# Kernel tuning notes

Measured on AMD Instinct MI355X. Metric: run time of the kernel, lower is better.

## Reference

```python
import jax, jax.numpy as jnp
import numpy as np

NUM_HEADS = 8


def setup_inputs() -> dict:
    key = jax.random.key(0)
    k1, k2, k3 = jax.random.split(key, 3)
    B, N, C = 4, 8448, 512
    x = jax.random.normal(k1, (B, N, C), dtype=jnp.float32)
    w_qkv = jax.random.normal(k2, (3 * C, C), dtype=jnp.float32) * (C ** -0.5)
    w_proj = jax.random.normal(k3, (C, C), dtype=jnp.float32) * (C ** -0.5)
    b_proj = jnp.zeros((C,), dtype=jnp.float32)
    return {"x": x, "w_qkv": w_qkv, "w_proj": w_proj, "b_proj": b_proj, "N_points": 8192}


def reference(x, w_qkv, w_proj, b_proj, N_points):
    B, N, C = x.shape
    H = NUM_HEADS
    hd = C // H
    scale = hd ** -0.5
    N_latent = N - N_points

    qkv = (x @ w_qkv.T).reshape(B, N, 3, H, hd).transpose(2, 0, 3, 1, 4)  # [3,B,H,N,hd]
    q, k, v = qkv[0], qkv[1], qkv[2]
    q_l, k_l, v_l = q[:, :, :N_latent], k[:, :, :N_latent], v[:, :, :N_latent]
    q_p, k_p, v_p = q[:, :, N_latent:], k[:, :, N_latent:], v[:, :, N_latent:]

    # joint cross+self attention for the points
    attn_cross = jnp.einsum('bhpd,bhld->bhpl', q_p, k_l) * scale        # [B,H,P,L]
    attn_self = jnp.sum(q_p * k_p, axis=-1, keepdims=True) * scale      # [B,H,P,1]
    attn_joint = jax.nn.softmax(jnp.concatenate([attn_cross, attn_self], axis=-1), axis=-1)

    sum_cross = jnp.einsum('bhpl,bhld->bhpd', attn_joint[..., :N_latent], v_l)
    sum_self = attn_joint[..., N_latent:] * v_p
    out_points = (sum_cross + sum_self).transpose(0, 2, 1, 3).reshape(B, N_points, C)

    # standard self-attention over latent tokens
    attn_latent = jax.nn.softmax(jnp.einsum('bhqd,bhkd->bhqk', q_l, k_l) * scale, axis=-1)
    out_latent = jnp.einsum('bhqk,bhkd->bhqd', attn_latent, v_l).transpose(0, 2, 1, 3).reshape(B, N_latent, C)

    output = jnp.concatenate([out_latent, out_points], axis=1) @ w_proj.T + b_proj
    attn_mean = attn_joint[..., :-1].mean(axis=1)  # [B,P,L]
    return output, attn_mean
```

## Files before the change

kernel.cpp:

```cpp
#include <hip/hip_runtime.h>

#define BQ 4
#define NH 8
#define NTOK 8448
#define NLAT 256
#define NPTS 8192
#define CDIM 512
#define HD 64
#define SCALE 0.125f

typedef __attribute__((ext_vector_type(8))) short short8b;
typedef __attribute__((ext_vector_type(4))) float f32x4;

static __device__ __forceinline__ float4 ld4(const float* p) { return *(const float4*)p; }

static __device__ __forceinline__ short f2b(float f) {
  union { float f; unsigned u; } c; c.f = f;
  unsigned u = c.u;
  u += ((u >> 16) & 1u) + 0x7fffu;
  return (short)(u >> 16);
}

static __device__ __forceinline__ float b2f(unsigned short u) {
  union { unsigned u; float f; } c; c.u = ((unsigned)u) << 16; return c.f;
}

static __device__ __forceinline__ int cvtpk(float lo, float hi) {
  int r; asm("v_cvt_pk_bf16_f32 %0, %1, %2" : "=v"(r) : "v"(lo), "v"(hi)); return r;
}

static __device__ __forceinline__ void gload_lds16(const unsigned short* g, unsigned short* l) {
  __builtin_amdgcn_global_load_lds((const __attribute__((address_space(1))) void*)g,
                                   (__attribute__((address_space(3))) void*)l, 16, 0, 0);
}

__global__ __launch_bounds__(256) void to_bf16_3(const float* __restrict__ a, unsigned short* __restrict__ ao_, int na8,
                                                 const float* __restrict__ b, unsigned short* __restrict__ bo, int nb8,
                                                 const float* __restrict__ c, unsigned short* __restrict__ co, int nc8) {
  int i = blockIdx.x * 256 + threadIdx.x;
  const float* src; unsigned short* dst; int idx;
  if (i < na8) { src = a; dst = ao_; idx = i; }
  else if (i < na8 + nb8) { src = b; dst = bo; idx = i - na8; }
  else if (i < na8 + nb8 + nc8) { src = c; dst = co; idx = i - na8 - nb8; }
  else return;
  float4 x0 = ld4(src + (size_t)idx * 8);
  float4 x1 = ld4(src + (size_t)idx * 8 + 4);
  short8b r;
  r[0] = f2b(x0.x); r[1] = f2b(x0.y); r[2] = f2b(x0.z); r[3] = f2b(x0.w);
  r[4] = f2b(x1.x); r[5] = f2b(x1.y); r[6] = f2b(x1.z); r[7] = f2b(x1.w);
  *(short8b*)&dst[(size_t)idx * 8] = r;
}

#define STAGE128(PA, PB, kt, s)                                                              \
  do {                                                                                       \
    const int _c = (kt) * 64 + scell;                                                        \
    unsigned short* _d = &lds[(s) * 16384 + t * 8];                                          \
    gload_lds16((PA) + (size_t)(m0 + sr) * CDIM + _c,       _d);                             \
    gload_lds16((PA) + (size_t)(m0 + 32 + sr) * CDIM + _c,  _d + 2048);                      \
    gload_lds16((PA) + (size_t)(m0 + 64 + sr) * CDIM + _c,  _d + 4096);                      \
    gload_lds16((PA) + (size_t)(m0 + 96 + sr) * CDIM + _c,  _d + 6144);                      \
    gload_lds16((PB) + (size_t)(j0 + sr) * CDIM + _c,       _d + 8192);                      \
    gload_lds16((PB) + (size_t)(j0 + 32 + sr) * CDIM + _c,  _d + 10240);                     \
    gload_lds16((PB) + (size_t)(j0 + 64 + sr) * CDIM + _c,  _d + 12288);                     \
    gload_lds16((PB) + (size_t)(j0 + 96 + sr) * CDIM + _c,  _d + 14336);                     \
  } while (0)

#define GEMM128_BODY(PA, PB)                                                                 \
  __shared__ unsigned short lds[32768];                                                      \
  const int fl = blockIdx.y * gridDim.x + blockIdx.x;                                        \
  const int nchunk = (gridDim.x * gridDim.y) >> 3;                                           \
  const int wid = (fl & 7) * nchunk + (fl >> 3);                                             \
  const int m0 = (wid / gridDim.x) * 128;                                                    \
  const int j0 = (wid % gridDim.x) * 128;                                                    \
  const int t = threadIdx.x;                                                                 \
  const int lane = t & 63, wave = t >> 6;                                                    \
  const int wr = wave >> 1, wc = wave & 1;                                                   \
  const int lm = lane & 15, lq = lane >> 4;                                                  \
  const int sr = t >> 3;                                    \
  const int scell = (((t & 7) ^ (sr & 7)) << 3);                                             \
  int offA[4], offB[4];                                                                      \
  _Pragma("unroll")                                                                          \
  for (int mt = 0; mt < 4; ++mt) {                                                           \
    const int RA = wr * 64 + mt * 16 + lm;                                                   \
    offA[mt] = RA * 64 + ((lq ^ (RA & 7)) << 3);                                             \
    const int RB = wc * 64 + mt * 16 + lm;                                                   \
    offB[mt] = 8192 + RB * 64 + ((lq ^ (RB & 7)) << 3);                                      \
  }                                                                                          \
  f32x4 acc[4][4] = {};                                                                      \
  STAGE128(PA, PB, 0, 0);                                                                    \
  STAGE128(PA, PB, 1, 1);                                                                    \
  for (int kt = 0; kt < 8; ++kt) {                                                           \
    const int s = kt & 1;                                                                    \
    if (kt == 7) asm volatile("s_waitcnt vmcnt(0)" ::: "memory");                            \
    else         asm volatile("s_waitcnt vmcnt(8)" ::: "memory");                            \
    __builtin_amdgcn_s_barrier();                                                            \
    const unsigned short* sb = &lds[s * 16384];                                              \
    short8b af[4][2], bf[4][2];                                                              \
    _Pragma("unroll")                                                                        \
    for (int mt = 0; mt < 4; ++mt) {                                                         \
      const int RA = wr * 64 + mt * 16 + lm;                                                 \
      const int RB = wc * 64 + mt * 16 + lm;                                                 \
      af[mt][0] = *(const short8b*)&sb[offA[mt]];                                            \
      af[mt][1] = *(const short8b*)&sb[(RA * 64) + (((4 | lq) ^ (RA & 7)) << 3)];            \
      bf[mt][0] = *(const short8b*)&sb[offB[mt]];                                            \
      bf[mt][1] = *(const short8b*)&sb[8192 + (RB * 64) + (((4 | lq) ^ (RB & 7)) << 3)];     \
    }                                                                                        \
    asm volatile("s_waitcnt lgkmcnt(0)" ::: "memory");                                       \
    __builtin_amdgcn_s_barrier();                                                            \
    __builtin_amdgcn_sched_barrier(0);                                                       \
    if (kt < 6) STAGE128(PA, PB, kt + 2, s);                                                 \
    __builtin_amdgcn_s_setprio(1);                                                           \
    _Pragma("unroll")                                                                        \
    for (int ks = 0; ks < 2; ++ks)                                                           \
      _Pragma("unroll")                                                                      \
      for (int mt = 0; mt < 4; ++mt)                                                         \
        _Pragma("unroll")                                                                    \
        for (int nt = 0; nt < 4; ++nt)                                                       \
          acc[mt][nt] = __builtin_amdgcn_mfma_f32_16x16x32_bf16(af[mt][ks], bf[nt][ks],      \
                                                                acc[mt][nt], 0, 0, 0);       \
    __builtin_amdgcn_s_setprio(0);                                                           \
  }

__global__ __launch_bounds__(256, 2) void qkv_mfma(const unsigned short* __restrict__ xb,
                                                   const unsigned short* __restrict__ wb,
                                                   unsigned short* __restrict__ qo,
                                                   unsigned short* __restrict__ ko,
                                                   unsigned short* __restrict__ vo) {
  GEMM128_BODY(xb, wb)
  const int s_ = j0 >> 9;
  unsigned short* dst = (s_ == 0) ? qo : ((s_ == 1) ? ko : vo);
  const int b = m0 / NTOK;
  const int n0 = m0 % NTOK;
  const int h = ((j0 >> 6) + wc) & 7;
#pragma unroll
  for (int mt = 0; mt < 4; ++mt) {
#pragma unroll
    for (int r = 0; r < 4; ++r) {
      const int n = n0 + wr * 64 + mt * 16 + lq * 4 + r;
      const size_t ob = (((size_t)b * NH + h) * NTOK + n) * HD;
#pragma unroll
      for (int nt = 0; nt < 4; ++nt)
        dst[ob + nt * 16 + lm] = (unsigned short)f2b(acc[mt][nt][r]);
    }
  }
}

__global__ __launch_bounds__(256, 2) void proj_mfma(const unsigned short* __restrict__ ab,
                                                    const unsigned short* __restrict__ wpb,
                                                    const float* __restrict__ bias,
                                                    float* __restrict__ out) {
  GEMM128_BODY(ab, wpb)
#pragma unroll
  for (int mt = 0; mt < 4; ++mt) {
#pragma unroll
    for (int r = 0; r < 4; ++r) {
      const int m = m0 + wr * 64 + mt * 16 + lq * 4 + r;
#pragma unroll
      for (int nt = 0; nt < 4; ++nt) {
        const int j = j0 + wc * 64 + nt * 16 + lm;
        out[(size_t)m * CDIM + j] = acc[mt][nt][r] + bias[j];
      }
    }
  }
}

__global__ __launch_bounds__(512, 2) void points_attn_mfma(const unsigned short* __restrict__ qb,
                                                           const unsigned short* __restrict__ kb,
                                                           const unsigned short* __restrict__ vb,
                                                           unsigned short* __restrict__ aob,
                                                           float* __restrict__ md) {
  __shared__ unsigned short kl[64 * 256];
  __shared__ unsigned short vt[64 * 256];
  const int fl = blockIdx.x;
  const int wid = (fl & 7) * 128 + (fl >> 3);
  const int bh = wid >> 5;
  const int ptile = wid & 31;
  const int t = threadIdx.x;
  const int lane = t & 63, wave = t >> 6;
  const int lm = lane & 15, lq = lane >> 4;
  const size_t bhb = (size_t)bh * NTOK * HD;
  if (t < 256) {
    const unsigned short* krg = kb + bhb + (size_t)t * HD;
    short8b kv[8];
#pragma unroll
    for (int i = 0; i < 8; ++i) kv[i] = *(const short8b*)(krg + i * 8);
    const int mtw = ((t >> 5) << 1) | ((t >> 2) & 1);
    const int lmw = (((t >> 3) & 3) << 2) | (t & 3);
    const int rr = (mtw << 4) | lmw;
#pragma unroll
    for (int j = 0; j < 8; ++j)
      *(short8b*)&kl[rr * 64 + ((j ^ (rr & 7)) << 3)] = kv[j];
  } else {
    const int tt = t - 256;
    const unsigned short* vr = vb + bhb + (size_t)tt * HD;
    short8b rv[8];
#pragma unroll
    for (int i = 0; i < 8; ++i) rv[i] = *(const short8b*)(vr + i * 8);
    const int gsw = tt >> 3, wi = tt & 7;
#pragma unroll
    for (int d0 = 0; d0 < 8; ++d0)
#pragma unroll
      for (int j = 0; j < 8; ++j)
        vt[(d0 * 8 + j) * 256 + ((gsw ^ j) << 3) + wi] = (unsigned short)rv[d0][j];
  }
  __syncthreads();
  const int b = bh >> 3, h = bh & 7;
#pragma unroll 1
  for (int pass = 0; pass < 2; ++pass) {
    const int pp0 = ptile * 256 + wave * 32 + pass * 16;
    const size_t qrow = bhb + (size_t)(NLAT + pp0 + lm) * HD;
    unsigned short vself[4][4];
#pragma unroll
    for (int ntd = 0; ntd < 4; ++ntd)
#pragma unroll
      for (int r = 0; r < 4; ++r)
        vself[ntd][r] = vb[bhb + (size_t)(NLAT + pp0 + lq * 4 + r) * HD + ntd * 16 + lm];
    const short8b bq0 = *(const short8b*)(qb + qrow + lq * 8);
    const short8b bq1 = *(const short8b*)(qb + qrow + 32 + lq * 8);
    f32x4 s[16] = {};
    __builtin_amdgcn_s_setprio(1);
#pragma unroll
    for (int mt = 0; mt < 16; ++mt) {
      const int rr = mt * 16 + lm;
      const short8b ak0 = *(const short8b*)&kl[rr * 64 + ((lq ^ (rr & 7)) << 3)];
      const short8b ak1 = *(const short8b*)&kl[rr * 64 + (((4 | lq) ^ (rr & 7)) << 3)];
      s[mt] = __builtin_amdgcn_mfma_f32_16x16x32_bf16(ak0, bq0, s[mt], 0, 0, 0);
      s[mt] = __builtin_amdgcn_mfma_f32_16x16x32_bf16(ak1, bq1, s[mt], 0, 0, 0);
    }
    __builtin_amdgcn_s_setprio(0);
    float sself = 0.f;
    {
      const unsigned short* qp = qb + qrow + lq * 16;
      const unsigned short* kp = kb + qrow + lq * 16;
      short8b q0 = *(const short8b*)qp, q1 = *(const short8b*)(qp + 8);
      short8b k0 = *(const short8b*)kp, k1 = *(const short8b*)(kp + 8);
#pragma unroll
      for (int j = 0; j < 8; ++j)
        sself += b2f((unsigned short)q0[j]) * b2f((unsigned short)k0[j]) +
                 b2f((unsigned short)q1[j]) * b2f((unsigned short)k1[j]);
    }
    sself += __shfl_xor(sself, 16);
    sself += __shfl_xor(sself, 32);
    sself *= SCALE;
    float mx = -1e30f;
#pragma unroll
    for (int mt = 0; mt < 16; ++mt)
#pragma unroll
      for (int r = 0; r < 4; ++r) mx = fmaxf(mx, s[mt][r]);
    mx = fmaxf(mx, __shfl_xor(mx, 16));
    mx = fmaxf(mx, __shfl_xor(mx, 32));
    const float m = fmaxf(mx * SCALE, sself);
    float sum = 0.f;
#pragma unroll
    for (int mt = 0; mt < 16; ++mt)
#pragma unroll
      for (int r = 0; r < 4; ++r) {
        float e = __expf(fmaf(s[mt][r], SCALE, -m));
        s[mt][r] = e;
        sum += e;
      }
    sum += __shfl_xor(sum, 16);
    sum += __shfl_xor(sum, 32);
    const float pself = __expf(sself - m);
    const float denom = sum + pself;
    if (lq == 0)
      *(float2*)&md[((size_t)bh * NPTS + pp0 + lm) * 2] = make_float2(m, denom);
    f32x4 o[4] = {};
    __builtin_amdgcn_s_setprio(1);
#pragma unroll
    for (int ks = 0; ks < 8; ++ks) {
      union { int i[4]; short8b v; } af;
      af.i[0] = cvtpk(s[2 * ks][0], s[2 * ks][1]);
      af.i[1] = cvtpk(s[2 * ks][2], s[2 * ks][3]);
      af.i[2] = cvtpk(s[2 * ks + 1][0], s[2 * ks + 1][1]);
      af.i[3] = cvtpk(s[2 * ks + 1][2], s[2 * ks + 1][3]);
#pragma unroll
      for (int ntd = 0; ntd < 4; ++ntd) {
        const int row = ntd * 16 + lm;
        const short8b bv = *(const short8b*)&vt[row * 256 + ((((ks << 2) | lq) ^ (lm & 7)) << 3)];
        o[ntd] = __builtin_amdgcn_mfma_f32_16x16x32_bf16(af.v, bv, o[ntd], 0, 0, 0);
      }
    }
    __builtin_amdgcn_s_setprio(0);
    float invd[4], psl[4];
#pragma unroll
    for (int r = 0; r < 4; ++r) {
      const int src = lq * 4 + r;
      invd[r] = 1.f / __shfl(denom, src);
      psl[r] = __shfl(pself, src);
    }
#pragma unroll
    for (int ntd = 0; ntd < 4; ++ntd) {
#pragma unroll
      for (int r = 0; r < 4; ++r) {
        const int n = NLAT + pp0 + lq * 4 + r;
        const float val = (o[ntd][r] + psl[r] * b2f(vself[ntd][r])) * invd[r];
        aob[((size_t)b * NTOK + n) * CDIM + h * HD + ntd * 16 + lm] = (unsigned short)f2b(val);
      }
    }
  }
}

__global__ __launch_bounds__(256) void latent_mfma(const unsigned short* __restrict__ qb,
                                                   const unsigned short* __restrict__ kb,
                                                   const unsigned short* __restrict__ vb,
                                                   unsigned short* __restrict__ aob) {
  __shared__ unsigned short vt[64 * 256];
  const int fl = blockIdx.x;
  const int wid = (fl & 7) * 16 + (fl >> 3);
  const int bh = wid >> 2;
  const int qt = wid & 3;
  const int t = threadIdx.x;
  const int lane = t & 63, wave = t >> 6;
  const int lm = lane & 15, lq = lane >> 4;
  const size_t bhb = (size_t)bh * NTOK * HD;
  {
    const unsigned short* vr = vb + bhb + (size_t)t * HD;
    short8b rv[8];
#pragma unroll
    for (int i = 0; i < 8; ++i) rv[i] = *(const short8b*)(vr + i * 8);
    const int gsw = t >> 3, wi = t & 7;
#pragma unroll
    for (int d0 = 0; d0 < 8; ++d0)
#pragma unroll
      for (int j = 0; j < 8; ++j)
        vt[(d0 * 8 + j) * 256 + ((gsw ^ j) << 3) + wi] = (unsigned short)rv[d0][j];
  }
  __syncthreads();
  const int b = bh >> 3, h = bh & 7;
  const int q0 = qt * 64 + wave * 16;
  const size_t qrow = bhb + (size_t)(q0 + lm) * HD;
  const short8b bq0 = *(const short8b*)(qb + qrow + lq * 8);
  const short8b bq1 = *(const short8b*)(qb + qrow + 32 + lq * 8);
  f32x4 s[16] = {};
  __builtin_amdgcn_s_setprio(1);
#pragma unroll
  for (int mt = 0; mt < 16; ++mt) {
    const int krow = ((mt >> 1) << 5) + ((lm >> 2) << 3) + ((mt & 1) << 2) + (lm & 3);
    const unsigned short* kr = kb + bhb + (size_t)krow * HD + lq * 8;
    s[mt] = __builtin_amdgcn_mfma_f32_16x16x32_bf16(*(const short8b*)kr, bq0, s[mt], 0, 0, 0);
    s[mt] = __builtin_amdgcn_mfma_f32_16x16x32_bf16(*(const short8b*)(kr + 32), bq1, s[mt], 0, 0, 0);
  }
  __builtin_amdgcn_s_setprio(0);
  float mx = -1e30f;
#pragma unroll
  for (int mt = 0; mt < 16; ++mt)
#pragma unroll
    for (int r = 0; r < 4; ++r) mx = fmaxf(mx, s[mt][r]);
  mx = fmaxf(mx, __shfl_xor(mx, 16));
  mx = fmaxf(mx, __shfl_xor(mx, 32));
  const float m = mx * SCALE;
  float sum = 0.f;
#pragma unroll
  for (int mt = 0; mt < 16; ++mt)
#pragma unroll
    for (int r = 0; r < 4; ++r) {
      float e = __expf(fmaf(s[mt][r], SCALE, -m));
      s[mt][r] = e;
      sum += e;
    }
  sum += __shfl_xor(sum, 16);
  sum += __shfl_xor(sum, 32);
  const float denom = sum;
  f32x4 o[4] = {};
  __builtin_amdgcn_s_setprio(1);
#pragma unroll
  for (int ks = 0; ks < 8; ++ks) {
    union { int i[4]; short8b v; } af;
    af.i[0] = cvtpk(s[2 * ks][0], s[2 * ks][1]);
    af.i[1] = cvtpk(s[2 * ks][2], s[2 * ks][3]);
    af.i[2] = cvtpk(s[2 * ks + 1][0], s[2 * ks + 1][1]);
    af.i[3] = cvtpk(s[2 * ks + 1][2], s[2 * ks + 1][3]);
#pragma unroll
    for (int ntd = 0; ntd < 4; ++ntd) {
      const int row = ntd * 16 + lm;
      const short8b bv = *(const short8b*)&vt[row * 256 + ((((ks << 2) | lq) ^ (lm & 7)) << 3)];
      o[ntd] = __builtin_amdgcn_mfma_f32_16x16x32_bf16(af.v, bv, o[ntd], 0, 0, 0);
    }
  }
  __builtin_amdgcn_s_setprio(0);
  float invd[4];
#pragma unroll
  for (int r = 0; r < 4; ++r) invd[r] = 1.f / __shfl(denom, lq * 4 + r);
#pragma unroll
  for (int ntd = 0; ntd < 4; ++ntd) {
#pragma unroll
    for (int r = 0; r < 4; ++r) {
      const int n = q0 + lq * 4 + r;
      aob[((size_t)b * NTOK + n) * CDIM + h * HD + ntd * 16 + lm] =
          (unsigned short)f2b(o[ntd][r] * invd[r]);
    }
  }
}

__global__ __launch_bounds__(256) void attn_mean_mfma(const unsigned short* __restrict__ qb,
                                                      const unsigned short* __restrict__ kb,
                                                      const float* __restrict__ md,
                                                      float* __restrict__ out1) {
  const int fl = blockIdx.x;
  const int wid = (fl & 7) * 64 + (fl >> 3);
  const int b = wid >> 7, pt = wid & 127;
  const int p0 = pt * 64;
  const int lane = threadIdx.x & 63;
  const int wave = threadIdx.x >> 6;
  const int n0 = wave * 64;
  const int lm = lane & 15, lq = lane >> 4;
  f32x4 prob[4][4] = {};
  for (int h = 0; h < NH; ++h) {
    const int bh = b * NH + h;
    const size_t qbase = ((size_t)bh * NTOK + NLAT + p0) * HD;
    const size_t kbase = (size_t)bh * NTOK * HD;
    f32x4 s[4][4] = {};
    __builtin_amdgcn_s_setprio(1);
#pragma unroll
    for (int kk = 0; kk < 2; ++kk) {
      const int dof = kk * 32 + lq * 8;
      short8b a[4], bb[4];
#pragma unroll
      for (int mt = 0; mt < 4; ++mt)
        a[mt] = *(const short8b*)(qb + qbase + (size_t)(mt * 16 + lm) * HD + dof);
#pragma unroll
      for (int nt = 0; nt < 4; ++nt)
        bb[nt] = *(const short8b*)(kb + kbase + (size_t)(n0 + nt * 16 + lm) * HD + dof);
#pragma unroll
      for (int mt = 0; mt < 4; ++mt)
#pragma unroll
        for (int nt = 0; nt < 4; ++nt)
          s[mt][nt] = __builtin_amdgcn_mfma_f32_16x16x32_bf16(a[mt], bb[nt], s[mt][nt], 0, 0, 0);
    }
    __builtin_amdgcn_s_setprio(0);
#pragma unroll
    for (int mt = 0; mt < 4; ++mt) {
#pragma unroll
      for (int r = 0; r < 4; ++r) {
        const int p = p0 + mt * 16 + lq * 4 + r;
        const float2 mv = *(const float2*)&md[((size_t)bh * NPTS + p) * 2];
        const float mm = mv.x;
        const float inv = __builtin_amdgcn_rcpf(mv.y);
#pragma unroll
        for (int nt = 0; nt < 4; ++nt)
          prob[mt][nt][r] += __expf(fmaf(s[mt][nt][r], SCALE, -mm)) * inv;
      }
    }
  }
#pragma unroll
  for (int mt = 0; mt < 4; ++mt) {
#pragma unroll
    for (int r = 0; r < 4; ++r) {
      const int p = p0 + mt * 16 + lq * 4 + r;
      const size_t ob = ((size_t)b * NPTS + p) * NLAT;
#pragma unroll
      for (int nt = 0; nt < 4; ++nt)
        out1[ob + n0 + nt * 16 + lm] = prob[mt][nt][r] * 0.125f;
    }
  }
}

extern "C" void kernel_launch(void* const* d_in, const int* in_sizes, int n_in,
                              void* d_out, int out_size, void* d_ws, size_t ws_size,
                              hipStream_t stream) {
  const float* x      = (const float*)d_in[0];
  const float* w_qkv  = (const float*)d_in[1];
  const float* w_proj = (const float*)d_in[2];
  const float* b_proj = (const float*)d_in[3];
  const size_t QSZ = (size_t)BQ * NH * NTOK * HD;
  unsigned short* qb  = (unsigned short*)d_ws;
  unsigned short* kb  = qb + QSZ;
  unsigned short* vb  = kb + QSZ;
  unsigned short* aob = vb + QSZ;
  unsigned short* xb  = aob + QSZ;
  unsigned short* wb  = xb + QSZ;
  unsigned short* wpb = wb + 786432;
  float* md = (float*)(wpb + 262144 + 128);
  float* out0 = (float*)d_out;
  float* out1 = out0 + (size_t)BQ * NTOK * CDIM;

  to_bf16_3<<<8960, 256, 0, stream>>>(x, xb, 2162688, w_qkv, wb, 98304, w_proj, wpb, 32768);
  qkv_mfma<<<dim3(12, 264), 256, 0, stream>>>(xb, wb, qb, kb, vb);
  points_attn_mfma<<<1024, 512, 0, stream>>>(qb, kb, vb, aob, md);
  latent_mfma<<<128, 256, 0, stream>>>(qb, kb, vb, aob);
  attn_mean_mfma<<<512, 256, 0, stream>>>(qb, kb, md, out1);
  proj_mfma<<<dim3(4, 264), 256, 0, stream>>>(aob, wpb, b_proj, out0);
}
```

Baseline: 226.0 us.

## Merge latent attention into points kernel, reorder GEMM prefetch, halve attn_mean tiles

Three separate changes. The latent self-attention kernel is folded into the points-attention launch as 64 extra blocks of 512 threads, so one launch covers both and the small latent grid can run alongside the larger one. The GEMM main loop now issues the next-stage global-to-LDS prefetch after the MFMA block rather than before it, and drops the precomputed LDS offsets. The attn_mean kernel now handles 32 points per block instead of 64, doubling its grid to 1024 blocks, which improves occupancy but re-reads K more often.

```diff
diff --git a/kernel.cpp b/kernel.cpp
--- a/kernel.cpp
+++ b/kernel.cpp
@@ -76,16 +76,8 @@
   const int lane = t & 63, wave = t >> 6;                                                    \
   const int wr = wave >> 1, wc = wave & 1;                                                   \
   const int lm = lane & 15, lq = lane >> 4;                                                  \
-  const int sr = t >> 3;                                    \
+  const int sr = t >> 3;                                                                     \
   const int scell = (((t & 7) ^ (sr & 7)) << 3);                                             \
-  int offA[4], offB[4];                                                                      \
-  _Pragma("unroll")                                                                          \
-  for (int mt = 0; mt < 4; ++mt) {                                                           \
-    const int RA = wr * 64 + mt * 16 + lm;                                                   \
-    offA[mt] = RA * 64 + ((lq ^ (RA & 7)) << 3);                                             \
-    const int RB = wc * 64 + mt * 16 + lm;                                                   \
-    offB[mt] = 8192 + RB * 64 + ((lq ^ (RB & 7)) << 3);                                      \
-  }                                                                                          \
   f32x4 acc[4][4] = {};                                                                      \
   STAGE128(PA, PB, 0, 0);                                                                    \
   STAGE128(PA, PB, 1, 1);                                                                    \
@@ -100,15 +92,11 @@
     for (int mt = 0; mt < 4; ++mt) {                                                         \
       const int RA = wr * 64 + mt * 16 + lm;                                                 \
       const int RB = wc * 64 + mt * 16 + lm;                                                 \
-      af[mt][0] = *(const short8b*)&sb[offA[mt]];                                            \
-      af[mt][1] = *(const short8b*)&sb[(RA * 64) + (((4 | lq) ^ (RA & 7)) << 3)];            \
-      bf[mt][0] = *(const short8b*)&sb[offB[mt]];                                            \
-      bf[mt][1] = *(const short8b*)&sb[8192 + (RB * 64) + (((4 | lq) ^ (RB & 7)) << 3)];     \
+      af[mt][0] = *(const short8b*)&sb[RA * 64 + ((lq ^ (RA & 7)) << 3)];                    \
+      af[mt][1] = *(const short8b*)&sb[RA * 64 + (((4 | lq) ^ (RA & 7)) << 3)];              \
+      bf[mt][0] = *(const short8b*)&sb[8192 + RB * 64 + ((lq ^ (RB & 7)) << 3)];             \
+      bf[mt][1] = *(const short8b*)&sb[8192 + RB * 64 + (((4 | lq) ^ (RB & 7)) << 3)];       \
     }                                                                                        \
-    asm volatile("s_waitcnt lgkmcnt(0)" ::: "memory");                                       \
-    __builtin_amdgcn_s_barrier();                                                            \
-    __builtin_amdgcn_sched_barrier(0);                                                       \
-    if (kt < 6) STAGE128(PA, PB, kt + 2, s);                                                 \
     __builtin_amdgcn_s_setprio(1);                                                           \
     _Pragma("unroll")                                                                        \
     for (int ks = 0; ks < 2; ++ks)                                                           \
@@ -119,6 +107,10 @@
           acc[mt][nt] = __builtin_amdgcn_mfma_f32_16x16x32_bf16(af[mt][ks], bf[nt][ks],      \
                                                                 acc[mt][nt], 0, 0, 0);       \
     __builtin_amdgcn_s_setprio(0);                                                           \
+    asm volatile("s_waitcnt lgkmcnt(0)" ::: "memory");                                       \
+    __builtin_amdgcn_s_barrier();                                                            \
+    __builtin_amdgcn_sched_barrier(0);                                                       \
+    if (kt < 6) STAGE128(PA, PB, kt + 2, s);                                                 \
   }
 
 __global__ __launch_bounds__(256, 2) void qkv_mfma(const unsigned short* __restrict__ xb,
@@ -164,84 +156,174 @@
   }
 }
 
-__global__ __launch_bounds__(512, 2) void points_attn_mfma(const unsigned short* __restrict__ qb,
-                                                           const unsigned short* __restrict__ kb,
-                                                           const unsigned short* __restrict__ vb,
-                                                           unsigned short* __restrict__ aob,
-                                                           float* __restrict__ md) {
+__global__ __launch_bounds__(512, 2) void attn_fused(const unsigned short* __restrict__ qb,
+                                                     const unsigned short* __restrict__ kb,
+                                                     const unsigned short* __restrict__ vb,
+                                                     unsigned short* __restrict__ aob,
+                                                     float* __restrict__ md) {
   __shared__ unsigned short kl[64 * 256];
   __shared__ unsigned short vt[64 * 256];
-  const int fl = blockIdx.x;
-  const int wid = (fl & 7) * 128 + (fl >> 3);
-  const int bh = wid >> 5;
-  const int ptile = wid & 31;
   const int t = threadIdx.x;
   const int lane = t & 63, wave = t >> 6;
   const int lm = lane & 15, lq = lane >> 4;
-  const size_t bhb = (size_t)bh * NTOK * HD;
-  if (t < 256) {
-    const unsigned short* krg = kb + bhb + (size_t)t * HD;
-    short8b kv[8];
-#pragma unroll
-    for (int i = 0; i < 8; ++i) kv[i] = *(const short8b*)(krg + i * 8);
-    const int mtw = ((t >> 5) << 1) | ((t >> 2) & 1);
-    const int lmw = (((t >> 3) & 3) << 2) | (t & 3);
-    const int rr = (mtw << 4) | lmw;
-#pragma unroll
-    for (int j = 0; j < 8; ++j)
-      *(short8b*)&kl[rr * 64 + ((j ^ (rr & 7)) << 3)] = kv[j];
+  if (blockIdx.x < 1024) {
+    const int fl = blockIdx.x;
+    const int wid = (fl & 7) * 128 + (fl >> 3);
+    const int bh = wid >> 5;
+    const int ptile = wid & 31;
+    const size_t bhb = (size_t)bh * NTOK * HD;
+    if (t < 256) {
+      const unsigned short* krg = kb + bhb + (size_t)t * HD;
+      short8b kv[8];
+#pragma unroll
+      for (int i = 0; i < 8; ++i) kv[i] = *(const short8b*)(krg + i * 8);
+      const int mtw = ((t >> 5) << 1) | ((t >> 2) & 1);
+      const int lmw = (((t >> 3) & 3) << 2) | (t & 3);
+      const int rr = (mtw << 4) | lmw;
+#pragma unroll
+      for (int j = 0; j < 8; ++j)
+        *(short8b*)&kl[rr * 64 + ((j ^ (rr & 7)) << 3)] = kv[j];
+    } else {
+      const int tt = t - 256;
+      const unsigned short* vr = vb + bhb + (size_t)tt * HD;
+      short8b rv[8];
+#pragma unroll
+      for (int i = 0; i < 8; ++i) rv[i] = *(const short8b*)(vr + i * 8);
+      const int gsw = tt >> 3, wi = tt & 7;
+#pragma unroll
+      for (int d0 = 0; d0 < 8; ++d0)
+#pragma unroll
+        for (int j = 0; j < 8; ++j)
+          vt[(d0 * 8 + j) * 256 + ((gsw ^ j) << 3) + wi] = (unsigned short)rv[d0][j];
+    }
+    __syncthreads();
+    const int b = bh >> 3, h = bh & 7;
+#pragma unroll 1
+    for (int pass = 0; pass < 2; ++pass) {
+      const int pp0 = ptile * 256 + wave * 32 + pass * 16;
+      const size_t qrow = bhb + (size_t)(NLAT + pp0 + lm) * HD;
+      unsigned short vself[4][4];
+#pragma unroll
+      for (int ntd = 0; ntd < 4; ++ntd)
+#pragma unroll
+        for (int r = 0; r < 4; ++r)
+          vself[ntd][r] = vb[bhb + (size_t)(NLAT + pp0 + lq * 4 + r) * HD + ntd * 16 + lm];
+      const short8b bq0 = *(const short8b*)(qb + qrow + lq * 8);
+      const short8b bq1 = *(const short8b*)(qb + qrow + 32 + lq * 8);
+      f32x4 s[16] = {};
+      __builtin_amdgcn_s_setprio(1);
+#pragma unroll
+      for (int mt = 0; mt < 16; ++mt) {
+        const int rr = mt * 16 + lm;
+        const short8b ak0 = *(const short8b*)&kl[rr * 64 + ((lq ^ (rr & 7)) << 3)];
+        const short8b ak1 = *(const short8b*)&kl[rr * 64 + (((4 | lq) ^ (rr & 7)) << 3)];
+        s[mt] = __builtin_amdgcn_mfma_f32_16x16x32_bf16(ak0, bq0, s[mt], 0, 0, 0);
+        s[mt] = __builtin_amdgcn_mfma_f32_16x16x32_bf16(ak1, bq1, s[mt], 0, 0, 0);
+      }
+      __builtin_amdgcn_s_setprio(0);
+      float sself = 0.f;
+      {
+        const unsigned short* qp = qb + qrow + lq * 16;
+        const unsigned short* kp = kb + qrow + lq * 16;
+        short8b q0 = *(const short8b*)qp, q1 = *(const short8b*)(qp + 8);
+        short8b k0 = *(const short8b*)kp, k1 = *(const short8b*)(kp + 8);
+#pragma unroll
+        for (int j = 0; j < 8; ++j)
+          sself += b2f((unsigned short)q0[j]) * b2f((unsigned short)k0[j]) +
+                   b2f((unsigned short)q1[j]) * b2f((unsigned short)k1[j]);
+      }
+      sself += __shfl_xor(sself, 16);
+      sself += __shfl_xor(sself, 32);
+      sself *= SCALE;
+      float mx = -1e30f;
+#pragma unroll
+      for (int mt = 0; mt < 16; ++mt)
+#pragma unroll
+        for (int r = 0; r < 4; ++r) mx = fmaxf(mx, s[mt][r]);
+      mx = fmaxf(mx, __shfl_xor(mx, 16));
+      mx = fmaxf(mx, __shfl_xor(mx, 32));
+      const float m = fmaxf(mx * SCALE, sself);
+      float sum = 0.f;
+#pragma unroll
+      for (int mt = 0; mt < 16; ++mt)
+#pragma unroll
+        for (int r = 0; r < 4; ++r) {
+          float e = __expf(fmaf(s[mt][r], SCALE, -m));
+          s[mt][r] = e;
+          sum += e;
+        }
+      sum += __shfl_xor(sum, 16);
+      sum += __shfl_xor(sum, 32);
+      const float pself = __expf(sself - m);
+      const float denom = sum + pself;
+      if (lq == 0)
+        *(float2*)&md[((size_t)bh * NPTS + pp0 + lm) * 2] = make_float2(m, denom);
+      f32x4 o[4] = {};
+      __builtin_amdgcn_s_setprio(1);
+#pragma unroll
+      for (int ks = 0; ks < 8; ++ks) {
+        union { int i[4]; short8b v; } af;
+        af.i[0] = cvtpk(s[2 * ks][0], s[2 * ks][1]);
+        af.i[1] = cvtpk(s[2 * ks][2], s[2 * ks][3]);
+        af.i[2] = cvtpk(s[2 * ks + 1][0], s[2 * ks + 1][1]);
+        af.i[3] = cvtpk(s[2 * ks + 1][2], s[2 * ks + 1][3]);
+#pragma unroll
+        for (int ntd = 0; ntd < 4; ++ntd) {
+          const int row = ntd * 16 + lm;
+          const short8b bv = *(const short8b*)&vt[row * 256 + ((((ks << 2) | lq) ^ (lm & 7)) << 3)];
+          o[ntd] = __builtin_amdgcn_mfma_f32_16x16x32_bf16(af.v, bv, o[ntd], 0, 0, 0);
+        }
+      }
+      __builtin_amdgcn_s_setprio(0);
+      float invd[4], psl[4];
+#pragma unroll
+      for (int r = 0; r < 4; ++r) {
+        const int src = lq * 4 + r;
+        invd[r] = 1.f / __shfl(denom, src);
+        psl[r] = __shfl(pself, src);
+      }
+#pragma unroll
+      for (int ntd = 0; ntd < 4; ++ntd) {
+#pragma unroll
+        for (int r = 0; r < 4; ++r) {
+          const int n = NLAT + pp0 + lq * 4 + r;
+          const float val = (o[ntd][r] + psl[r] * b2f(vself[ntd][r])) * invd[r];
+          aob[((size_t)b * NTOK + n) * CDIM + h * HD + ntd * 16 + lm] = (unsigned short)f2b(val);
+        }
+      }
+    }
   } else {
-    const int tt = t - 256;
-    const unsigned short* vr = vb + bhb + (size_t)tt * HD;
-    short8b rv[8];
-#pragma unroll
-    for (int i = 0; i < 8; ++i) rv[i] = *(const short8b*)(vr + i * 8);
-    const int gsw = tt >> 3, wi = tt & 7;
-#pragma unroll
-    for (int d0 = 0; d0 < 8; ++d0)
-#pragma unroll
-      for (int j = 0; j < 8; ++j)
-        vt[(d0 * 8 + j) * 256 + ((gsw ^ j) << 3) + wi] = (unsigned short)rv[d0][j];
-  }
-  __syncthreads();
-  const int b = bh >> 3, h = bh & 7;
-#pragma unroll 1
-  for (int pass = 0; pass < 2; ++pass) {
-    const int pp0 = ptile * 256 + wave * 32 + pass * 16;
-    const size_t qrow = bhb + (size_t)(NLAT + pp0 + lm) * HD;
-    unsigned short vself[4][4];
-#pragma unroll
-    for (int ntd = 0; ntd < 4; ++ntd)
-#pragma unroll
-      for (int r = 0; r < 4; ++r)
-        vself[ntd][r] = vb[bhb + (size_t)(NLAT + pp0 + lq * 4 + r) * HD + ntd * 16 + lm];
+    const int idx = blockIdx.x - 1024;
+    const int bh = idx >> 1, half = idx & 1;
+    const size_t bhb = (size_t)bh * NTOK * HD;
+    if (t < 256) {
+      const unsigned short* vr = vb + bhb + (size_t)t * HD;
+      short8b rv[8];
+#pragma unroll
+      for (int i = 0; i < 8; ++i) rv[i] = *(const short8b*)(vr + i * 8);
+      const int gsw = t >> 3, wi = t & 7;
+#pragma unroll
+      for (int d0 = 0; d0 < 8; ++d0)
+#pragma unroll
+        for (int j = 0; j < 8; ++j)
+          vt[(d0 * 8 + j) * 256 + ((gsw ^ j) << 3) + wi] = (unsigned short)rv[d0][j];
+    }
+    __syncthreads();
+    const int b = bh >> 3, h = bh & 7;
+    const int q0 = half * 128 + wave * 16;
+    const size_t qrow = bhb + (size_t)(q0 + lm) * HD;
     const short8b bq0 = *(const short8b*)(qb + qrow + lq * 8);
     const short8b bq1 = *(const short8b*)(qb + qrow + 32 + lq * 8);
     f32x4 s[16] = {};
     __builtin_amdgcn_s_setprio(1);
 #pragma unroll
     for (int mt = 0; mt < 16; ++mt) {
-      const int rr = mt * 16 + lm;
-      const short8b ak0 = *(const short8b*)&kl[rr * 64 + ((lq ^ (rr & 7)) << 3)];
-      const short8b ak1 = *(const short8b*)&kl[rr * 64 + (((4 | lq) ^ (rr & 7)) << 3)];
-      s[mt] = __builtin_amdgcn_mfma_f32_16x16x32_bf16(ak0, bq0, s[mt], 0, 0, 0);
-      s[mt] = __builtin_amdgcn_mfma_f32_16x16x32_bf16(ak1, bq1, s[mt], 0, 0, 0);
+      const int krow = ((mt >> 1) << 5) + ((lm >> 2) << 3) + ((mt & 1) << 2) + (lm & 3);
+      const unsigned short* kr = kb + bhb + (size_t)krow * HD + lq * 8;
+      s[mt] = __builtin_amdgcn_mfma_f32_16x16x32_bf16(*(const short8b*)kr, bq0, s[mt], 0, 0, 0);
+      s[mt] = __builtin_amdgcn_mfma_f32_16x16x32_bf16(*(const short8b*)(kr + 32), bq1, s[mt], 0, 0, 0);
     }
     __builtin_amdgcn_s_setprio(0);
-    float sself = 0.f;
-    {
-      const unsigned short* qp = qb + qrow + lq * 16;
-      const unsigned short* kp = kb + qrow + lq * 16;
-      short8b q0 = *(const short8b*)qp, q1 = *(const short8b*)(qp + 8);
-      short8b k0 = *(const short8b*)kp, k1 = *(const short8b*)(kp + 8);
-#pragma unroll
-      for (int j = 0; j < 8; ++j)
-        sself += b2f((unsigned short)q0[j]) * b2f((unsigned short)k0[j]) +
-                 b2f((unsigned short)q1[j]) * b2f((unsigned short)k1[j]);
-    }
-    sself += __shfl_xor(sself, 16);
-    sself += __shfl_xor(sself, 32);
-    sself *= SCALE;
     float mx = -1e30f;
 #pragma unroll
     for (int mt = 0; mt < 16; ++mt)
@@ -249,7 +331,7 @@
       for (int r = 0; r < 4; ++r) mx = fmaxf(mx, s[mt][r]);
     mx = fmaxf(mx, __shfl_xor(mx, 16));
     mx = fmaxf(mx, __shfl_xor(mx, 32));
-    const float m = fmaxf(mx * SCALE, sself);
+    const float m = mx * SCALE;
     float sum = 0.f;
 #pragma unroll
     for (int mt = 0; mt < 16; ++mt)
@@ -261,10 +343,7 @@
       }
     sum += __shfl_xor(sum, 16);
     sum += __shfl_xor(sum, 32);
-    const float pself = __expf(sself - m);
-    const float denom = sum + pself;
-    if (lq == 0)
-      *(float2*)&md[((size_t)bh * NPTS + pp0 + lm) * 2] = make_float2(m, denom);
+    const float denom = sum;
     f32x4 o[4] = {};
     __builtin_amdgcn_s_setprio(1);
 #pragma unroll
@@ -282,113 +361,17 @@
       }
     }
     __builtin_amdgcn_s_setprio(0);
-    float invd[4], psl[4];
-#pragma unroll
-    for (int r = 0; r < 4; ++r) {
-      const int src = lq * 4 + r;
-      invd[r] = 1.f / __shfl(denom, src);
-      psl[r] = __shfl(pself, src);
-    }
+    float invd[4];
+#pragma unroll
+    for (int r = 0; r < 4; ++r) invd[r] = 1.f / __shfl(denom, lq * 4 + r);
 #pragma unroll
     for (int ntd = 0; ntd < 4; ++ntd) {
 #pragma unroll
       for (int r = 0; r < 4; ++r) {
-        const int n = NLAT + pp0 + lq * 4 + r;
-        const float val = (o[ntd][r] + psl[r] * b2f(vself[ntd][r])) * invd[r];
-        aob[((size_t)b * NTOK + n) * CDIM + h * HD + ntd * 16 + lm] = (unsigned short)f2b(val);
-      }
-    }
-  }
-}
-
-__global__ __launch_bounds__(256) void latent_mfma(const unsigned short* __restrict__ qb,
-                                                   const unsigned short* __restrict__ kb,
-                                                   const unsigned short* __restrict__ vb,
-                                                   unsigned short* __restrict__ aob) {
-  __shared__ unsigned short vt[64 * 256];
-  const int fl = blockIdx.x;
-  const int wid = (fl & 7) * 16 + (fl >> 3);
-  const int bh = wid >> 2;
-  const int qt = wid & 3;
-  const int t = threadIdx.x;
-  const int lane = t & 63, wave = t >> 6;
-  const int lm = lane & 15, lq = lane >> 4;
-  const size_t bhb = (size_t)bh * NTOK * HD;
-  {
-    const unsigned short* vr = vb + bhb + (size_t)t * HD;
-    short8b rv[8];
-#pragma unroll
-    for (int i = 0; i < 8; ++i) rv[i] = *(const short8b*)(vr + i * 8);
-    const int gsw = t >> 3, wi = t & 7;
-#pragma unroll
-    for (int d0 = 0; d0 < 8; ++d0)
-#pragma unroll
-      for (int j = 0; j < 8; ++j)
-        vt[(d0 * 8 + j) * 256 + ((gsw ^ j) << 3) + wi] = (unsigned short)rv[d0][j];
-  }
-  __syncthreads();
-  const int b = bh >> 3, h = bh & 7;
-  const int q0 = qt * 64 + wave * 16;
-  const size_t qrow = bhb + (size_t)(q0 + lm) * HD;
-  const short8b bq0 = *(const short8b*)(qb + qrow + lq * 8);
-  const short8b bq1 = *(const short8b*)(qb + qrow + 32 + lq * 8);
-  f32x4 s[16] = {};
-  __builtin_amdgcn_s_setprio(1);
-#pragma unroll
-  for (int mt = 0; mt < 16; ++mt) {
-    const int krow = ((mt >> 1) << 5) + ((lm >> 2) << 3) + ((mt & 1) << 2) + (lm & 3);
-    const unsigned short* kr = kb + bhb + (size_t)krow * HD + lq * 8;
-    s[mt] = __builtin_amdgcn_mfma_f32_16x16x32_bf16(*(const short8b*)kr, bq0, s[mt], 0, 0, 0);
-    s[mt] = __builtin_amdgcn_mfma_f32_16x16x32_bf16(*(const short8b*)(kr + 32), bq1, s[mt], 0, 0, 0);
-  }
-  __builtin_amdgcn_s_setprio(0);
-  float mx = -1e30f;
-#pragma unroll
-  for (int mt = 0; mt < 16; ++mt)
-#pragma unroll
-    for (int r = 0; r < 4; ++r) mx = fmaxf(mx, s[mt][r]);
-  mx = fmaxf(mx, __shfl_xor(mx, 16));
-  mx = fmaxf(mx, __shfl_xor(mx, 32));
-  const float m = mx * SCALE;
-  float sum = 0.f;
-#pragma unroll
-  for (int mt = 0; mt < 16; ++mt)
-#pragma unroll
-    for (int r = 0; r < 4; ++r) {
-      float e = __expf(fmaf(s[mt][r], SCALE, -m));
-      s[mt][r] = e;
-      sum += e;
-    }
-  sum += __shfl_xor(sum, 16);
-  sum += __shfl_xor(sum, 32);
-  const float denom = sum;
-  f32x4 o[4] = {};
-  __builtin_amdgcn_s_setprio(1);
-#pragma unroll
-  for (int ks = 0; ks < 8; ++ks) {
-    union { int i[4]; short8b v; } af;
-    af.i[0] = cvtpk(s[2 * ks][0], s[2 * ks][1]);
-    af.i[1] = cvtpk(s[2 * ks][2], s[2 * ks][3]);
-    af.i[2] = cvtpk(s[2 * ks + 1][0], s[2 * ks + 1][1]);
-    af.i[3] = cvtpk(s[2 * ks + 1][2], s[2 * ks + 1][3]);
-#pragma unroll
-    for (int ntd = 0; ntd < 4; ++ntd) {
-      const int row = ntd * 16 + lm;
-      const short8b bv = *(const short8b*)&vt[row * 256 + ((((ks << 2) | lq) ^ (lm & 7)) << 3)];
-      o[ntd] = __builtin_amdgcn_mfma_f32_16x16x32_bf16(af.v, bv, o[ntd], 0, 0, 0);
-    }
-  }
-  __builtin_amdgcn_s_setprio(0);
-  float invd[4];
-#pragma unroll
-  for (int r = 0; r < 4; ++r) invd[r] = 1.f / __shfl(denom, lq * 4 + r);
-#pragma unroll
-  for (int ntd = 0; ntd < 4; ++ntd) {
-#pragma unroll
-    for (int r = 0; r < 4; ++r) {
-      const int n = q0 + lq * 4 + r;
-      aob[((size_t)b * NTOK + n) * CDIM + h * HD + ntd * 16 + lm] =
-          (unsigned short)f2b(o[ntd][r] * invd[r]);
+        const int n = q0 + lq * 4 + r;
+        aob[((size_t)b * NTOK + n) * CDIM + h * HD + ntd * 16 + lm] =
+            (unsigned short)f2b(o[ntd][r] * invd[r]);
+      }
     }
   }
 }
@@ -398,39 +381,39 @@
                                                       const float* __restrict__ md,
                                                       float* __restrict__ out1) {
   const int fl = blockIdx.x;
-  const int wid = (fl & 7) * 64 + (fl >> 3);
-  const int b = wid >> 7, pt = wid & 127;
-  const int p0 = pt * 64;
+  const int wid = (fl & 7) * 128 + (fl >> 3);
+  const int b = wid >> 8, pt = wid & 255;
+  const int p0 = pt * 32;
   const int lane = threadIdx.x & 63;
   const int wave = threadIdx.x >> 6;
   const int n0 = wave * 64;
   const int lm = lane & 15, lq = lane >> 4;
-  f32x4 prob[4][4] = {};
+  f32x4 prob[2][4] = {};
   for (int h = 0; h < NH; ++h) {
     const int bh = b * NH + h;
     const size_t qbase = ((size_t)bh * NTOK + NLAT + p0) * HD;
     const size_t kbase = (size_t)bh * NTOK * HD;
-    f32x4 s[4][4] = {};
+    f32x4 s[2][4] = {};
     __builtin_amdgcn_s_setprio(1);
 #pragma unroll
     for (int kk = 0; kk < 2; ++kk) {
       const int dof = kk * 32 + lq * 8;
-      short8b a[4], bb[4];
-#pragma unroll
-      for (int mt = 0; mt < 4; ++mt)
+      short8b a[2], bb[4];
+#pragma unroll
+      for (int mt = 0; mt < 2; ++mt)
         a[mt] = *(const short8b*)(qb + qbase + (size_t)(mt * 16 + lm) * HD + dof);
 #pragma unroll
       for (int nt = 0; nt < 4; ++nt)
         bb[nt] = *(const short8b*)(kb + kbase + (size_t)(n0 + nt * 16 + lm) * HD + dof);
 #pragma unroll
-      for (int mt = 0; mt < 4; ++mt)
+      for (int mt = 0; mt < 2; ++mt)
 #pragma unroll
         for (int nt = 0; nt < 4; ++nt)
           s[mt][nt] = __builtin_amdgcn_mfma_f32_16x16x32_bf16(a[mt], bb[nt], s[mt][nt], 0, 0, 0);
     }
     __builtin_amdgcn_s_setprio(0);
 #pragma unroll
-    for (int mt = 0; mt < 4; ++mt) {
+    for (int mt = 0; mt < 2; ++mt) {
 #pragma unroll
       for (int r = 0; r < 4; ++r) {
         const int p = p0 + mt * 16 + lq * 4 + r;
@@ -444,7 +427,7 @@
     }
   }
 #pragma unroll
-  for (int mt = 0; mt < 4; ++mt) {
+  for (int mt = 0; mt < 2; ++mt) {
 #pragma unroll
     for (int r = 0; r < 4; ++r) {
       const int p = p0 + mt * 16 + lq * 4 + r;
@@ -477,8 +460,7 @@
 
   to_bf16_3<<<8960, 256, 0, stream>>>(x, xb, 2162688, w_qkv, wb, 98304, w_proj, wpb, 32768);
   qkv_mfma<<<dim3(12, 264), 256, 0, stream>>>(xb, wb, qb, kb, vb);
-  points_attn_mfma<<<1024, 512, 0, stream>>>(qb, kb, vb, aob, md);
-  latent_mfma<<<128, 256, 0, stream>>>(qb, kb, vb, aob);
-  attn_mean_mfma<<<512, 256, 0, stream>>>(qb, kb, md, out1);
+  attn_fused<<<1088, 512, 0, stream>>>(qb, kb, vb, aob, md);
+  attn_mean_mfma<<<1024, 256, 0, stream>>>(qb, kb, md, out1);
   proj_mfma<<<dim3(4, 264), 256, 0, stream>>>(aob, wpb, b_proj, out0);
 }
```

Measured after the change: 254.6 us. 1.13x slower.
